# Kernel tuning notes

Measured on AMD Instinct MI355X. Metric: run time of the kernel, lower is better.

## Reference

```python
import jax, jax.numpy as jnp
import numpy as np

H = 768        # spanbert_out
WF = 20        # width_encoding_feature_size
MSW = 10       # max_span_width
TOP_RATIO = 0.4
MAX_ANTE = 50
DEPTH = 2      # coref_depth
D = 3 * H + WF # span_rep_size = 2324
NEG = -1e30


def setup_inputs() -> dict:
    key = jax.random.key(0)
    ks = jax.random.split(key, 12)
    W, G = 2048, 100
    seq = jax.random.normal(ks[0], (W, H), jnp.float32)
    sentence_map = jnp.sort(jax.random.randint(ks[1], (W,), 0, 64))
    gold_starts = jax.random.randint(ks[2], (G,), 0, W)
    gold_ends = jnp.clip(gold_starts + jax.random.randint(ks[3], (G,), 0, MSW), 0, W - 1)
    cluster_ids = jax.random.randint(ks[4], (G,), 0, 20)
    s = 0.02
    return {
        "sequence_output": seq,
        "W_alpha": jax.random.normal(ks[5], (H, 1), jnp.float32) * s,
        "b_alpha": jnp.zeros((1,), jnp.float32),
        "W_m": jax.random.normal(ks[6], (D, 1), jnp.float32) * s,
        "b_m": jnp.zeros((1,), jnp.float32),
        "W_c": jax.random.normal(ks[7], (D, D), jnp.float32) * s,
        "W_a": jax.random.normal(ks[8], (3 * D, 1), jnp.float32) * s,
        "b_a": jnp.zeros((1,), jnp.float32),
        "W_f": jax.random.normal(ks[9], (2 * D, D), jnp.float32) * s,
        "b_f": jnp.zeros((D,), jnp.float32),
        "width_feats": jax.random.normal(ks[10], (MSW, WF), jnp.float32) * s,
        "sentence_map": sentence_map,
        "gold_starts": gold_starts,
        "gold_ends": gold_ends,
        "cluster_ids": cluster_ids,
    }


def _forward(seq, W_alpha, b_alpha, W_m, b_m, W_c, W_a, b_a, W_f, b_f, width_feats,
             sentence_map, gold_starts, gold_ends, cluster_ids):
    W = seq.shape[0]
    # candidate spans: [W, MSW] -> flat [N], N = W*MSW
    cs = jnp.broadcast_to(jnp.arange(W)[:, None], (W, MSW)).reshape(-1)
    ce = (jnp.arange(W)[:, None] + jnp.arange(MSW)[None, :]).reshape(-1)
    ce_c = jnp.minimum(ce, W - 1)
    valid = (ce < W) & (sentence_map[cs] == sentence_map[ce_c])  # [N]

    # candidate cluster labels (get_candidate_labels): sum cluster ids of exact gold matches
    same_span = (cs[:, None] == gold_starts[None, :]) & (ce_c[:, None] == gold_ends[None, :])
    cand_cluster = jnp.sum(jnp.where(same_span, cluster_ids[None, :], 0), axis=1)  # [N]

    # span representations
    start_emb = seq[cs]                               # [N,H]
    end_emb = seq[ce_c]                               # [N,H]
    alphas = (seq @ W_alpha + b_alpha)[:, 0]          # [W]
    doc_range = jnp.arange(W)[None, :]
    mmask = (doc_range >= cs[:, None]) & (doc_range <= ce_c[:, None])  # [N,W]
    attn = jax.nn.softmax(jnp.where(mmask, alphas[None, :], NEG), axis=1)
    span_emb = attn @ seq                             # [N,H]
    widths = jnp.clip(ce_c - cs, 0, MSW - 1)          # width - 1
    rep = jnp.concatenate([start_emb, end_emb, span_emb, width_feats[widths]], axis=1)  # [N,D]

    # mention scoring + top-m pruning (masked_select replaced by -inf masking)
    mention_scores = (rep @ W_m + b_m)[:, 0]          # [N]
    masked_scores = jnp.where(valid, mention_scores, NEG)
    m = int(TOP_RATIO * W)
    _, top_idx = jax.lax.top_k(masked_scores, m)
    top_idx = jnp.sort(top_idx)
    top_rep = rep[top_idx]                            # [m,D]
    ts, te = cs[top_idx], ce_c[top_idx]
    tscore = mention_scores[top_idx]
    tcluster = cand_cluster[top_idx]

    # prune antecedents
    k = min(m, MAX_ANTE)
    offsets = jnp.arange(m)[:, None] - jnp.arange(m)[None, :]
    amask = offsets >= 1
    fast = tscore[:, None] + tscore[None, :] + jnp.where(amask, 0.0, NEG)
    fast = fast + (top_rep @ W_c) @ top_rep.T         # [m,m]
    _, top_ante = jax.lax.top_k(fast, k)              # [m,k]
    ta_mask = jnp.take_along_axis(amask, top_ante, axis=1)
    ta_fast = jnp.take_along_axis(fast, top_ante, axis=1)

    # iterative attention-weighted antecedent aggregation with gated update
    dummy = jnp.zeros((m, 1), seq.dtype)
    reps = top_rep
    scores_a = ta_fast
    for _ in range(DEPTH):
        ante_emb = reps[top_ante]                     # [m,k,D]
        tgt = reps[:, None, :]
        pair = jnp.concatenate(
            [jnp.broadcast_to(tgt, (m, k, D)), ante_emb, ante_emb * tgt], axis=2)  # [m,k,3D]
        slow = (pair @ W_a)[:, :, 0] + b_a[0]         # [m,k]
        scores_a = ta_fast + slow
        wts = jax.nn.softmax(jnp.concatenate([dummy, scores_a], axis=1), axis=1)  # [m,k+1]
        full = jnp.concatenate([reps[:, None, :], ante_emb], axis=1)              # [m,k+1,D]
        attended = jnp.sum(wts[:, :, None] * full, axis=1)                        # [m,D]
        f = jax.nn.sigmoid(jnp.concatenate([reps, attended], axis=1) @ W_f + b_f)
        reps = f * attended + (1.0 - f) * reps

    final_scores = jnp.concatenate([dummy, scores_a], axis=1)  # [m,k+1]

    # antecedent labels and marginal log-likelihood loss
    ante_cluster = jnp.where(ta_mask, tcluster[top_ante], -1)
    pairwise = (ante_cluster == tcluster[:, None]) & (tcluster > 0)[:, None]
    dummy_lab = ~jnp.any(pairwise, axis=1, keepdims=True)
    lab = jnp.concatenate([dummy_lab, pairwise], axis=1)
    gold_scores = jnp.where(lab, final_scores, NEG)
    loss = jnp.sum(jax.nn.logsumexp(final_scores, axis=1) - jax.nn.logsumexp(gold_scores, axis=1))
    return ts, te, top_ante, final_scores, loss


def reference(sequence_output, W_alpha, b_alpha, W_m, b_m, W_c, W_a, b_a, W_f, b_f,
              width_feats, sentence_map, gold_starts, gold_ends, cluster_ids):
    return _forward(sequence_output, W_alpha, b_alpha, W_m, b_m, W_c, W_a, b_a,
                    W_f, b_f, width_feats, sentence_map, gold_starts, gold_ends, cluster_ids)
```

## Files before the change

kernel.cpp:

```cpp
#include <hip/hip_runtime.h>
#include <cfloat>
#include <climits>
#include <math.h>

#define HD   768
#define MSW  10
#define WFK  20
#define DD   2324
#define K2   50
#define NEGF (-1e30f)

#define KPAD 2432
#define KAW  4864
#define MPAD 896
#define NPAD 2432

typedef __attribute__((ext_vector_type(8))) short    s8b;
typedef __attribute__((ext_vector_type(8))) unsigned short u16x8;
typedef __attribute__((ext_vector_type(4))) float    f32x4;

__device__ inline unsigned short f2bf(float f){
  unsigned u = __float_as_uint(f);
  unsigned r = (u + 0x7FFFu + ((u >> 16) & 1u)) >> 16;
  return (unsigned short)r;
}
__device__ inline float bf2f(unsigned short h){
  return __uint_as_float(((unsigned)h) << 16);
}

__device__ __forceinline__ void gload16(const unsigned short* g, void* l){
  __builtin_amdgcn_global_load_lds(
      (const __attribute__((address_space(1))) void*)g,
      (__attribute__((address_space(3))) void*)l, 16, 0, 0);
}

__device__ __forceinline__ int swz_col(int row, int col){
  return col ^ ((row & 7) << 3);
}

__global__ void row_proj(const float* __restrict__ seq, const float* __restrict__ Wa,
                         const float* __restrict__ ba, const float* __restrict__ Wm,
                         float* alphas, float* p1, float* p2, float* p3, int W){
  int w = blockIdx.x; int tid = threadIdx.x;
  const float* row = seq + (size_t)w * HD;
  float s0=0.f, s1=0.f, s2=0.f, s3=0.f;
  for(int h=tid; h<HD; h+=256){
    float x = row[h];
    s0 += x * Wa[h];
    s1 += x * Wm[h];
    s2 += x * Wm[HD + h];
    s3 += x * Wm[2*HD + h];
  }
  __shared__ float r0[256], r1[256], r2[256], r3[256];
  r0[tid]=s0; r1[tid]=s1; r2[tid]=s2; r3[tid]=s3;
  __syncthreads();
  for(int st=128; st>0; st>>=1){
    if(tid<st){ r0[tid]+=r0[tid+st]; r1[tid]+=r1[tid+st]; r2[tid]+=r2[tid+st]; r3[tid]+=r3[tid+st]; }
    __syncthreads();
  }
  if(tid==0){ alphas[w]=r0[0]+ba[0]; p1[w]=r1[0]; p2[w]=r2[0]; p3[w]=r3[0]; }
}

__global__ void mention_kernel(const float* __restrict__ alphas, const float* __restrict__ p1,
                               const float* __restrict__ p2, const float* __restrict__ p3,
                               const float* __restrict__ wfeat, const float* __restrict__ Wm,
                               const float* __restrict__ bm,
                               const int* __restrict__ smap, const int* __restrict__ gs,
                               const int* __restrict__ ge, const int* __restrict__ cid, int G,
                               float* mscore, float* mmask, int* ccl, int W){
  int c = blockIdx.x*blockDim.x + threadIdx.x;
  int C = W * MSW;
  if(c >= C) return;
  int s = c / MSW, r = c - s*MSW;
  int e = s + r; int ec = min(e, W-1);
  int L = ec - s;
  bool valid = (e < W) && (smap[s] == smap[ec]);
  float maxa = -FLT_MAX;
  for(int j=0;j<=L;j++) maxa = fmaxf(maxa, alphas[s+j]);
  float sum=0.f, sdot=0.f;
  for(int j=0;j<=L;j++){ float ee = expf(alphas[s+j]-maxa); sum += ee; sdot += ee*p3[s+j]; }
  sdot /= sum;
  float wp=0.f;
  for(int f=0; f<WFK; f++) wp += wfeat[L*WFK+f] * Wm[3*HD+f];
  float ms = p1[s] + p2[ec] + sdot + wp + bm[0];
  mscore[c] = ms;
  mmask[c]  = valid ? ms : NEGF;
  int cc = 0;
  for(int g=0; g<G; g++) if(s==gs[g] && ec==ge[g]) cc += cid[g];
  ccl[c] = cc;
}

__device__ inline unsigned fkey(float f){
  unsigned b = __float_as_uint(f);
  return (b & 0x80000000u) ? ~b : (b | 0x80000000u);
}

__global__ __launch_bounds__(1024)
void select_kernel(const float* __restrict__ mmask, const float* __restrict__ mscore,
                   const int* __restrict__ ccl, int m, int C, int W,
                   int* top_idx, float* tscore, int* tclust,
                   float* out_ts, float* out_te){
  const int T = 1024;
  int tid = threadIdx.x;
  int chunk = (C + T - 1)/T;
  int lo = tid*chunk, hi = min(lo+chunk, C);
  int n = hi - lo; if(n < 0) n = 0;
  unsigned kb[32];
  for(int t=0;t<n;t++) kb[t] = fkey(mmask[lo+t]);

  __shared__ unsigned s_hist[256];
  __shared__ unsigned s_scan[1024];
  __shared__ unsigned s_pref;
  __shared__ int s_rem;
  if(tid==0){ s_pref=0u; s_rem=m; }
  __syncthreads();

  for(int b=3;b>=0;b--){
    if(tid<256) s_hist[tid]=0u;
    __syncthreads();
    unsigned pref = s_pref;
    unsigned msk = (b==3)?0u:(0xFFFFFFFFu << ((b+1)*8));
    for(int t=0;t<n;t++){
      unsigned u = kb[t];
      if((u & msk)==pref) atomicAdd(&s_hist[(u>>(b*8))&0xFFu], 1u);
    }
    __syncthreads();
    if(tid==0){
      int rem = s_rem; unsigned acc=0u; int bin;
      for(bin=255;bin>=1;bin--){
        unsigned h = s_hist[bin];
        if(acc + h >= (unsigned)rem) break;
        acc += h;
      }
      if(bin < 0) bin = 0;
      s_pref = pref | ((unsigned)bin << (b*8));
      s_rem = rem - (int)acc;
    }
    __syncthreads();
  }
  unsigned Tk = s_pref;
  int need = s_rem;

  unsigned nG=0, nE=0;
  for(int t=0;t<n;t++){ unsigned u=kb[t]; nG += (u>Tk)?1u:0u; nE += (u==Tk)?1u:0u; }

  s_scan[tid]=nE; __syncthreads();
  for(int off=1; off<T; off<<=1){
    unsigned x = (tid>=off)? s_scan[tid-off]:0u; __syncthreads();
    s_scan[tid]+=x; __syncthreads();
  }
  unsigned eqBase = s_scan[tid]-nE;
  __syncthreads();

  int takeLeft = need - (int)eqBase;
  int take = takeLeft<0?0:(takeLeft>(int)nE?(int)nE:takeLeft);
  unsigned selCnt = nG + (unsigned)take;

  s_scan[tid]=selCnt; __syncthreads();
  for(int off=1; off<T; off<<=1){
    unsigned x = (tid>=off)? s_scan[tid-off]:0u; __syncthreads();
    s_scan[tid]+=x; __syncthreads();
  }
  unsigned posBase = s_scan[tid]-selCnt;

  int pos = (int)posBase; int eq = (int)eqBase;
  for(int t=0;t<n;t++){
    unsigned u = kb[t];
    bool sel = false;
    if(u>Tk) sel=true;
    else if(u==Tk){ if(eq<need) sel=true; eq++; }
    if(sel){
      int c = lo+t;
      top_idx[pos] = c;
      int s = c/MSW, r = c - s*MSW; int e = min(s + r, W-1);
      tscore[pos] = mscore[c];
      tclust[pos] = ccl[c];
      out_ts[pos] = (float)s;
      out_te[pos] = (float)e;
      pos++;
    }
  }
}

__global__ void build_rep(const float* __restrict__ seq, const float* __restrict__ alphas,
                          const float* __restrict__ wfeat, const int* __restrict__ top_idx,
                          float* rep, int W){
  int i = blockIdx.x; int tid = threadIdx.x;
  int c = top_idx[i];
  int s = c/MSW, r = c - s*MSW; int ec = min(s + r, W-1); int L = ec - s;
  float wv[MSW];
  float maxa = -FLT_MAX;
  for(int j=0;j<=L;j++) maxa = fmaxf(maxa, alphas[s+j]);
  float sum = 0.f;
  for(int j=0;j<=L;j++){ wv[j] = expf(alphas[s+j]-maxa); sum += wv[j]; }
  float inv = 1.f/sum;
  float* o = rep + (size_t)i*DD;
  for(int d=tid; d<HD; d+=256){
    o[d]      = seq[(size_t)s*HD + d];
    o[HD+d]   = seq[(size_t)ec*HD + d];
    float sp = 0.f;
    for(int j=0;j<=L;j++) sp += wv[j]*seq[(size_t)(s+j)*HD + d];
    o[2*HD+d] = sp*inv;
  }
  for(int f=tid; f<WFK; f+=256) o[3*HD+f] = wfeat[L*WFK+f];
}

__global__ void zero_buf(float* __restrict__ p, int n){
  int i = blockIdx.x*256 + threadIdx.x;
  if(i < n) p[i] = 0.f;
}

__global__ void conv_split(const float* __restrict__ src, int rows, int cols,
                           unsigned short* __restrict__ hi, unsigned short* __restrict__ lo){
  int idx = blockIdx.x*256 + threadIdx.x;
  if(idx >= MPAD*KPAD) return;
  int row = idx / KPAD, col = idx - row*KPAD;
  float v = (row < rows && col < cols) ? src[(size_t)row*cols + col] : 0.f;
  unsigned short h = f2bf(v);
  int w = row*KPAD + swz_col(row, col);
  hi[w] = h;
  lo[w] = f2bf(v - bf2f(h));
}

__global__ void conv_split_wcT(const float* __restrict__ Wc,
                               unsigned short* __restrict__ WtH, unsigned short* __restrict__ WtL){
  int n  = blockIdx.y*64 + threadIdx.x;
  int k8 = blockIdx.x*8;
  u16x8 vh, vl;
  #pragma unroll
  for(int j=0;j<8;j++){
    int k = k8 + j;
    float f = (n < DD && k < DD) ? Wc[(size_t)k*DD + n] : 0.f;
    unsigned short h = f2bf(f);
    vh[j] = h;
    vl[j] = f2bf(f - bf2f(h));
  }
  int k8s = swz_col(n, k8);
  *(u16x8*)(WtH + (size_t)n*KPAD + k8s) = vh;
  *(u16x8*)(WtL + (size_t)n*KPAD + k8s) = vl;
}

__global__ void conv_slow_ops(const float* __restrict__ cur, const float* __restrict__ Wa3,
                              unsigned short* __restrict__ CurBf, unsigned short* __restrict__ Xbf,
                              int m){
  int idx = blockIdx.x*256 + threadIdx.x;
  if(idx >= MPAD*KPAD) return;
  int row = idx / KPAD, col = idx - row*KPAD;
  float v = 0.f, w = 0.f;
  if(row < m && col < DD){ v = cur[(size_t)row*DD + col]; w = Wa3[2*DD + col]; }
  int ws = row*KPAD + swz_col(row, col);
  CurBf[ws] = f2bf(v);
  Xbf[ws]   = f2bf(v * w);
}

__global__ __launch_bounds__(256,2)
void gemm_split3_sk(const unsigned short* __restrict__ Ah, const unsigned short* __restrict__ Al,
                    const unsigned short* __restrict__ Bth, const unsigned short* __restrict__ Btl,
                    float* __restrict__ C, int M, int N, int ldc){
  __shared__ __align__(16) unsigned short sAh[128*64];
  __shared__ __align__(16) unsigned short sAl[128*64];
  __shared__ __align__(16) unsigned short sBh[128*64];
  __shared__ __align__(16) unsigned short sBl[128*64];
  int t = threadIdx.x;
  int row0 = blockIdx.y*128, col0 = blockIdx.x*128;
  const int tiles = KPAD/64;
  int per = (tiles + (int)gridDim.z - 1)/(int)gridDim.z;
  int tb = min((int)blockIdx.z*per, tiles), te = min(tb + per, tiles);
  if(tb >= te) return;
  int lane = t&63, w = t>>6;
  int wr = (w>>1)*64, wc = (w&1)*64;
  int quad = lane>>4, l15 = lane&15;
  int seg = lane&7;
  size_t ro = (size_t)(w*8 + (lane>>3));
  const unsigned short* gAh = Ah  + ((size_t)row0 + ro)*KPAD + seg*8;
  const unsigned short* gAl = Al  + ((size_t)row0 + ro)*KPAD + seg*8;
  const unsigned short* gBh = Bth + ((size_t)col0 + ro)*KPAD + seg*8;
  const unsigned short* gBl = Btl + ((size_t)col0 + ro)*KPAD + seg*8;
  const int lds0 = (w*8)*64;
  const int c0 = ((quad ^ (l15 & 7)) << 3);

  f32x4 acc[4][4];
  #pragma unroll
  for(int mi=0;mi<4;mi++)
    #pragma unroll
    for(int ni=0;ni<4;ni++) acc[mi][ni] = (f32x4){0.f,0.f,0.f,0.f};

  for(int kt=tb; kt<te; ++kt){
    size_t k0 = (size_t)kt*64;
    #pragma unroll
    for(int r=0;r<4;r++){
      size_t go = (size_t)(r*32)*KPAD + k0;
      int lo = lds0 + r*32*64;
      gload16(gAh + go, sAh + lo);
      gload16(gAl + go, sAl + lo);
      gload16(gBh + go, sBh + lo);
      gload16(gBl + go, sBl + lo);
    }
    __syncthreads();
    #pragma unroll
    for(int ks=0;ks<2;ks++){
      const int co = c0 ^ (ks<<5);
      s8b fah[4], fal[4], fbh[4], fbl[4];
      #pragma unroll
      for(int mi=0;mi<4;mi++){
        int ra = (wr+mi*16+l15)*64 + co;
        fah[mi] = *(const s8b*)&sAh[ra];
        fal[mi] = *(const s8b*)&sAl[ra];
      }
      #pragma unroll
      for(int ni=0;ni<4;ni++){
        int rb = (wc+ni*16+l15)*64 + co;
        fbh[ni] = *(const s8b*)&sBh[rb];
        fbl[ni] = *(const s8b*)&sBl[rb];
      }
      #pragma unroll
      for(int mi=0;mi<4;mi++)
        #pragma unroll
        for(int ni=0;ni<4;ni++){
          acc[mi][ni] = __builtin_amdgcn_mfma_f32_16x16x32_bf16(fah[mi], fbh[ni], acc[mi][ni], 0,0,0);
          acc[mi][ni] = __builtin_amdgcn_mfma_f32_16x16x32_bf16(fah[mi], fbl[ni], acc[mi][ni], 0,0,0);
          acc[mi][ni] = __builtin_amdgcn_mfma_f32_16x16x32_bf16(fal[mi], fbh[ni], acc[mi][ni], 0,0,0);
        }
    }
    __syncthreads();
  }

  #pragma unroll
  for(int ni=0;ni<4;ni++){
    int gn = col0 + wc + ni*16 + l15;
    if(gn >= N) continue;
    #pragma unroll
    for(int mi=0;mi<4;mi++){
      #pragma unroll
      for(int rg=0;rg<4;rg++){
        int gr = row0 + wr + mi*16 + quad*4 + rg;
        if(gr >= M) continue;
        atomicAdd(&C[(size_t)gr*ldc + gn], acc[mi][ni][rg]);
      }
    }
  }
}

__global__ __launch_bounds__(256,2)
void gemm_bf16_m97(const unsigned short* __restrict__ A, const unsigned short* __restrict__ Bt,
                   float* __restrict__ C, int M, int N, int ldc, int ldk, int tiles){
  __shared__ __align__(16) unsigned short sA[2][128*64];
  __shared__ __align__(16) unsigned short sB[2][128*64];
  int t = threadIdx.x;
  int row0 = blockIdx.y*128, col0 = blockIdx.x*128;
  int per = (tiles + (int)gridDim.z - 1)/(int)gridDim.z;
  int tb = min((int)blockIdx.z*per, tiles), te = min(tb + per, tiles);
  if(tb >= te) return;
  int lane = t&63, w = t>>6;
  int wr = (w>>1)*64, wc = (w&1)*64;
  int quad = lane>>4, l15 = lane&15;
  int seg = lane&7;
  size_t ro = (size_t)(w*8 + (lane>>3));
  const unsigned short* gA = A  + ((size_t)row0 + ro)*ldk + seg*8;
  const unsigned short* gB = Bt + ((size_t)col0 + ro)*ldk + seg*8;
  const int lds0 = (w*8)*64;
  const int c0 = ((quad ^ (l15 & 7)) << 3);

  f32x4 acc[4][4];
  #pragma unroll
  for(int mi=0;mi<4;mi++)
    #pragma unroll
    for(int ni=0;ni<4;ni++) acc[mi][ni] = (f32x4){0.f,0.f,0.f,0.f};

  auto STAGE = [&](int b, int kt){
    size_t k0 = (size_t)kt*64;
    #pragma unroll
    for(int r=0;r<4;r++){
      size_t go = (size_t)(r*32)*ldk + k0;
      int lo = lds0 + r*32*64;
      gload16(gA + go, &sA[b][lo]);
      gload16(gB + go, &sB[b][lo]);
    }
  };

  STAGE(0, tb);
  __syncthreads();
  int buf = 0;
  for(int kt=tb; kt<te; ++kt){
    if(kt+1 < te) STAGE(buf^1, kt+1);
    #pragma unroll
    for(int ks=0;ks<2;ks++){
      const int co = c0 ^ (ks<<5);
      s8b fa[4], fb[4];
      #pragma unroll
      for(int mi=0;mi<4;mi++) fa[mi] = *(const s8b*)&sA[buf][(wr+mi*16+l15)*64 + co];
      #pragma unroll
      for(int ni=0;ni<4;ni++) fb[ni] = *(const s8b*)&sB[buf][(wc+ni*16+l15)*64 + co];
      #pragma unroll
      for(int mi=0;mi<4;mi++)
        #pragma unroll
        for(int ni=0;ni<4;ni++)
          acc[mi][ni] = __builtin_amdgcn_mfma_f32_16x16x32_bf16(fa[mi], fb[ni], acc[mi][ni], 0,0,0);
    }
    __syncthreads();
    buf ^= 1;
  }

  #pragma unroll
  for(int ni=0;ni<4;ni++){
    int gn = col0 + wc + ni*16 + l15;
    if(gn >= N) continue;
    #pragma unroll
    for(int mi=0;mi<4;mi++){
      #pragma unroll
      for(int rg=0;rg<4;rg++){
        int gr = row0 + wr + mi*16 + quad*4 + rg;
        if(gr >= M) continue;
        atomicAdd(&C[(size_t)gr*ldc + gn], acc[mi][ni][rg]);
      }
    }
  }
}

#define NT 13
__global__ void topante_kernel(const float* __restrict__ tscore, const float* __restrict__ bilin,
                               int m, int* ante, float* tafast, float* out_ante){
  int i = blockIdx.x; int lane = threadIdx.x;
  float tsi = tscore[i];
  float v[NT];
  #pragma unroll
  for(int t=0;t<NT;t++){
    int j = lane + t*64;
    float f = -FLT_MAX;
    if(j < m){
      f = tsi + tscore[j];
      f += (j < i) ? 0.f : NEGF;
      f += bilin[(size_t)i*m + j];
    }
    v[t] = f;
  }
  unsigned consumed = 0u;
  int r_ante = 0; float r_fast = 0.f;
  for(int it=0; it<K2; ++it){
    float lv = -FLT_MAX; int li = m;
    #pragma unroll
    for(int t=0;t<NT;t++){
      bool live = ((consumed >> t) & 1u) == 0u;
      if(live && v[t] > lv){ lv = v[t]; li = lane + t*64; }
    }
    float bv = lv; int bi = li;
    #pragma unroll
    for(int off=32; off>0; off>>=1){
      float ov = __shfl_xor(bv, off);
      int   oi = __shfl_xor(bi, off);
      if(ov > bv || (ov == bv && oi < bi)){ bv = ov; bi = oi; }
    }
    if(bi < m && (bi & 63) == lane) consumed |= (1u << (bi >> 6));
    if(lane == it){ r_ante = bi; r_fast = bv; }
  }
  if(lane < K2){
    ante[(size_t)i*K2 + lane]   = r_ante;
    tafast[(size_t)i*K2 + lane] = r_fast;
    out_ante[(size_t)i*K2+lane] = (float)r_ante;
  }
}

__global__ void uv_kernel(const float* __restrict__ reps, const float* __restrict__ Wa3,
                          float* u, float* v, int m){
  int i = blockIdx.x; int tid = threadIdx.x;
  const float* rp = reps + (size_t)i*DD;
  float s1=0.f, s2=0.f;
  for(int d=tid; d<DD; d+=256){ float x = rp[d]; s1 += x*Wa3[d]; s2 += x*Wa3[DD+d]; }
  __shared__ float r1[256], r2[256];
  r1[tid]=s1; r2[tid]=s2; __syncthreads();
  for(int st=128; st>0; st>>=1){
    if(tid<st){ r1[tid]+=r1[tid+st]; r2[tid]+=r2[tid+st]; }
    __syncthreads();
  }
  if(tid==0){ u[i]=r1[0]; v[i]=r2[0]; }
}

__global__ void slow_gather(const float* __restrict__ P, const float* __restrict__ u,
                            const float* __restrict__ v, const int* __restrict__ ante,
                            const float* __restrict__ tafast, const float* __restrict__ ba,
                            float* sc, int m){
  int p = blockIdx.x*256 + threadIdx.x;
  if(p >= m*K2) return;
  int i = p / K2; int j = ante[p];
  sc[p] = tafast[p] + u[i] + v[j] + P[(size_t)i*m + j] + ba[0];
}

__global__ void attend_kernel(const float* __restrict__ reps, const float* __restrict__ sc,
                              const int* __restrict__ ante, float* att, int m){
  int i = blockIdx.x; int tid = threadIdx.x;
  __shared__ float wts[K2+1];
  __shared__ float scs[K2];
  __shared__ int   js[K2];
  if(tid < K2){ scs[tid] = sc[(size_t)i*K2 + tid]; js[tid] = ante[(size_t)i*K2 + tid]; }
  __syncthreads();
  if(tid==0){
    float mx = 0.f;
    for(int t=0;t<K2;t++) mx = fmaxf(mx, scs[t]);
    float sum = expf(0.f - mx); wts[0] = sum;
    for(int t=0;t<K2;t++){ float e = expf(scs[t]-mx); wts[t+1]=e; sum += e; }
    float inv = 1.f/sum;
    for(int t=0;t<=K2;t++) wts[t] *= inv;
  }
  __syncthreads();
  const float* ri_ = reps + (size_t)i*DD;
  for(int d=tid; d<DD; d+=256){
    float a = wts[0]*ri_[d];
    for(int t=0;t<K2;t++) a += wts[t+1]*reps[(size_t)js[t]*DD + d];
    att[(size_t)i*DD + d] = a;
  }
}

__global__ void conv_acat(const float* __restrict__ cur, const float* __restrict__ att,
                          unsigned short* __restrict__ A, int m){
  int idx = blockIdx.x*256 + threadIdx.x;
  if(idx >= MPAD*KAW) return;
  int row = idx / KAW, col = idx - row*KAW;
  float v = 0.f;
  if(row < m){
    if(col < DD) v = cur[(size_t)row*DD + col];
    else if(col >= KPAD && col < KPAD + DD) v = att[(size_t)row*DD + (col - KPAD)];
  }
  A[row*KAW + swz_col(row, col)] = f2bf(v);
}

__global__ void conv_wf(const float* __restrict__ Wf, unsigned short* __restrict__ Bt){
  int n  = blockIdx.y*64 + threadIdx.x;
  int k8 = blockIdx.x*8;
  int s  = (k8 >= KPAD) ? 1 : 0;
  int kk = k8 - s*KPAD;
  u16x8 v;
  #pragma unroll
  for(int j=0;j<8;j++){
    int k = kk + j;
    float f = (n < DD && k < DD) ? Wf[(size_t)(s*DD + k)*DD + n] : 0.f;
    v[j] = f2bf(f);
  }
  int k8s = swz_col(n, k8);
  *(u16x8*)(Bt + (size_t)n*KAW + k8s) = v;
}

__global__ void gate_update(const float* __restrict__ bfv, const float* __restrict__ att,
                            const float* __restrict__ cur, float* __restrict__ nxt, int total){
  int idx = blockIdx.x*256 + threadIdx.x;
  if(idx >= total) return;
  int col = idx % DD;
  float pre = nxt[idx] + bfv[col];
  float g = 1.f/(1.f + expf(-pre));
  nxt[idx] = g*att[idx] + (1.f - g)*cur[idx];
}

__global__ void final_loss(const float* __restrict__ sc, const int* __restrict__ ante,
                           const int* __restrict__ tclust, float* out_fs, float* row_loss, int m){
  int i = blockIdx.x*blockDim.x + threadIdx.x;
  if(i >= m) return;
  int tci = tclust[i];
  unsigned long long labm = 0ull;
  bool anyp = false;
  float mx = 0.f;
  float mg = -FLT_MAX;
  for(int t=0;t<K2;t++){
    float v = sc[(size_t)i*K2 + t];
    mx = fmaxf(mx, v);
    int j = ante[(size_t)i*K2 + t];
    bool mk = (j < i);
    int ac = mk ? tclust[j] : -1;
    bool p = (ac == tci) && (tci > 0);
    if(p){ labm |= (1ull << (t+1)); anyp = true; mg = fmaxf(mg, v); }
  }
  if(!anyp){ labm |= 1ull; mg = 0.f; }
  float s1 = expf(0.f - mx);
  float s2 = (labm & 1ull) ? expf(0.f - mg) : 0.f;
  float* o = out_fs + (size_t)i*(K2+1);
  o[0] = 0.f;
  for(int t=0;t<K2;t++){
    float v = sc[(size_t)i*K2 + t];
    o[t+1] = v;
    s1 += expf(v - mx);
    if(labm & (1ull << (t+1))) s2 += expf(v - mg);
  }
  row_loss[i] = (mx + logf(s1)) - (mg + logf(s2));
}

__global__ void loss_sum(const float* __restrict__ row_loss, float* out, int m){
  int tid = threadIdx.x;
  float s = 0.f;
  for(int i=tid; i<m; i+=256) s += row_loss[i];
  __shared__ float red[256];
  red[tid]=s; __syncthreads();
  for(int st=128; st>0; st>>=1){ if(tid<st) red[tid]+=red[tid+st]; __syncthreads(); }
  if(tid==0) out[0] = red[0];
}

extern "C" void kernel_launch(void* const* d_in, const int* in_sizes, int n_in,
                              void* d_out, int out_size, void* d_ws, size_t ws_size,
                              hipStream_t stream){
  const int W = in_sizes[11];
  const int G = in_sizes[12];
  const int C = W * MSW;
  const int m = (int)(0.4 * (double)W);

  const float* seq   = (const float*)d_in[0];
  const float* Wal   = (const float*)d_in[1];
  const float* bal   = (const float*)d_in[2];
  const float* Wm    = (const float*)d_in[3];
  const float* bm    = (const float*)d_in[4];
  const float* Wc    = (const float*)d_in[5];
  const float* WaA   = (const float*)d_in[6];
  const float* baA   = (const float*)d_in[7];
  const float* Wf    = (const float*)d_in[8];
  const float* bf    = (const float*)d_in[9];
  const float* wfeat = (const float*)d_in[10];
  const int*   smap  = (const int*)d_in[11];
  const int*   gs    = (const int*)d_in[12];
  const int*   ge    = (const int*)d_in[13];
  const int*   cid   = (const int*)d_in[14];
  float* out = (float*)d_out;

  char* ws = (char*)d_ws;
  size_t off = 0;
  auto alloc = [&](size_t bytes)->char*{
    char* p = ws + off;
    off += (bytes + 255) & ~(size_t)255;
    return p;
  };
  const size_t PLANE  = (size_t)MPAD*KPAD*2;
  const size_t WPLANE = (size_t)NPAD*KPAD*2;

  float* alphas  = (float*)alloc((size_t)W*4);
  float* p1      = (float*)alloc((size_t)W*4);
  float* p2      = (float*)alloc((size_t)W*4);
  float* p3      = (float*)alloc((size_t)W*4);
  float* mscore  = (float*)alloc((size_t)C*4);
  float* mmask   = (float*)alloc((size_t)C*4);
  int*   ccl     = (int*)  alloc((size_t)C*4);
  int*   top_idx = (int*)  alloc((size_t)m*4);
  float* tscore  = (float*)alloc((size_t)m*4);
  int*   tclust  = (int*)  alloc((size_t)m*4);
  float* B1      = (float*)alloc((size_t)m*DD*4);
  float* B2      = (float*)alloc((size_t)m*DD*4);
  float* B3      = (float*)alloc((size_t)m*DD*4);
  float* bilin   = (float*)alloc((size_t)m*m*4);
  int*   ante    = (int*)  alloc((size_t)m*K2*4);
  float* tafast  = (float*)alloc((size_t)m*K2*4);
  float* uB      = (float*)alloc((size_t)m*4);
  float* vB      = (float*)alloc((size_t)m*4);
  float* scB     = (float*)alloc((size_t)m*K2*4);
  float* rloss   = (float*)alloc((size_t)m*4);
  char* regionA = alloc(2*PLANE);
  unsigned short* RepH  = (unsigned short*)regionA;
  unsigned short* RepL  = (unsigned short*)(regionA + PLANE);
  unsigned short* XbfA  = (unsigned short*)regionA;
  unsigned short* CurBf = (unsigned short*)(regionA + PLANE);
  unsigned short* Acat  = (unsigned short*)regionA;
  char* regionB = alloc(2*WPLANE);
  unsigned short* WtH  = (unsigned short*)regionB;
  unsigned short* WtL  = (unsigned short*)(regionB + WPLANE);
  unsigned short* A2H  = (unsigned short*)regionB;
  unsigned short* A2L  = (unsigned short*)(regionB + PLANE);
  unsigned short* BtWf = (unsigned short*)regionB;

  float* out_ts   = out;
  float* out_te   = out + m;
  float* out_ante = out + 2*m;
  float* out_fs   = out + 2*m + (size_t)m*K2;
  float* out_loss = out + 2*m + (size_t)m*K2 + (size_t)m*(K2+1);

  row_proj<<<W, 256, 0, stream>>>(seq, Wal, bal, Wm, alphas, p1, p2, p3, W);
  mention_kernel<<<(C+255)/256, 256, 0, stream>>>(alphas, p1, p2, p3, wfeat, Wm, bm,
                                                  smap, gs, ge, cid, G,
                                                  mscore, mmask, ccl, W);
  select_kernel<<<1, 1024, 0, stream>>>(mmask, mscore, ccl, m, C, W,
                                        top_idx, tscore, tclust, out_ts, out_te);
  build_rep<<<m, 256, 0, stream>>>(seq, alphas, wfeat, top_idx, B1, W);
  {
    const int NEL = MPAD*KPAD;
    conv_split<<<(NEL+255)/256, 256, 0, stream>>>(B1, m, DD, RepH, RepL);
    dim3 gw(KPAD/8, NPAD/64);
    conv_split_wcT<<<gw, 64, 0, stream>>>(Wc, WtH, WtL);
    zero_buf<<<(m*DD+255)/256, 256, 0, stream>>>(B2, m*DD);
    dim3 g1(NPAD/128, MPAD/128, 3);
    gemm_split3_sk<<<g1, 256, 0, stream>>>(RepH, RepL, WtH, WtL, B2, m, DD, DD);
    conv_split<<<(NEL+255)/256, 256, 0, stream>>>(B2, m, DD, A2H, A2L);
    zero_buf<<<(m*m+255)/256, 256, 0, stream>>>(bilin, m*m);
    dim3 g2(MPAD/128, MPAD/128, 10);
    gemm_split3_sk<<<g2, 256, 0, stream>>>(A2H, A2L, RepH, RepL, bilin, m, m, m);
  }
  topante_kernel<<<m, 64, 0, stream>>>(tscore, bilin, m, ante, tafast, out_ante);
  {
    dim3 g(KAW/8, NPAD/64);
    conv_wf<<<g, 64, 0, stream>>>(Wf, BtWf);
  }

  float* cur = B1; float* nxt = B2;
  const int NEL = MPAD*KPAD;
  const int total = m * DD;
  for(int depth=0; depth<2; depth++){
    uv_kernel<<<m, 256, 0, stream>>>(cur, WaA, uB, vB, m);
    conv_slow_ops<<<(NEL+255)/256, 256, 0, stream>>>(cur, WaA, CurBf, XbfA, m);
    zero_buf<<<(m*m+255)/256, 256, 0, stream>>>(bilin, m*m);
    dim3 gp(MPAD/128, MPAD/128, 10);
    gemm_bf16_m97<<<gp, 256, 0, stream>>>(XbfA, CurBf, bilin, m, m, m, KPAD, KPAD/64);
    slow_gather<<<(m*K2+255)/256, 256, 0, stream>>>(bilin, uB, vB, ante, tafast, baA, scB, m);
    attend_kernel<<<m, 256, 0, stream>>>(cur, scB, ante, B3, m);
    conv_acat<<<(MPAD*KAW+255)/256, 256, 0, stream>>>(cur, B3, Acat, m);
    zero_buf<<<(total+255)/256, 256, 0, stream>>>(nxt, total);
    dim3 gg(NPAD/128, MPAD/128, 3);
    gemm_bf16_m97<<<gg, 256, 0, stream>>>(Acat, BtWf, nxt, m, DD, DD, KAW, KAW/64);
    gate_update<<<(total+255)/256, 256, 0, stream>>>(bf, B3, cur, nxt, total);
    float* t = cur; cur = nxt; nxt = t;
  }

  final_loss<<<(m+255)/256, 256, 0, stream>>>(scB, ante, tclust, out_fs, rloss, m);
  loss_sum<<<1, 256, 0, stream>>>(rloss, out_loss, m);
}
```

Before: 843.2 us.

## Double-buffer split-bf16 GEMM LDS tiles with 32-wide K and new swizzle

Splits the K tile from 64 to 32 and double-buffers the LDS staging, so the async global-to-LDS loads for the next tile are issued before the MFMA work on the current one. The LDS swizzle and the matching operand conversion kernels change to a 32-column pattern. This aims to hide global load latency behind compute, at the cost of twice as many loop iterations and barriers, and possible LDS bank conflicts if the new swizzle does not spread the accesses well. Only one barrier per iteration remains, so correctness depends on the async loads completing before that barrier.

```diff
diff --git a/kernel.cpp b/kernel.cpp
--- a/kernel.cpp
+++ b/kernel.cpp
@@ -36,6 +36,9 @@
 
 __device__ __forceinline__ int swz_col(int row, int col){
   return col ^ ((row & 7) << 3);
+}
+__device__ __forceinline__ int swz32(int row, int col){
+  return col ^ (((row >> 1) & 3) << 3);
 }
 
 __global__ void row_proj(const float* __restrict__ seq, const float* __restrict__ Wa,
@@ -217,7 +220,7 @@
   int row = idx / KPAD, col = idx - row*KPAD;
   float v = (row < rows && col < cols) ? src[(size_t)row*cols + col] : 0.f;
   unsigned short h = f2bf(v);
-  int w = row*KPAD + swz_col(row, col);
+  int w = row*KPAD + swz32(row, col);
   hi[w] = h;
   lo[w] = f2bf(v - bf2f(h));
 }
@@ -235,7 +238,7 @@
     vh[j] = h;
     vl[j] = f2bf(f - bf2f(h));
   }
-  int k8s = swz_col(n, k8);
+  int k8s = swz32(n, k8);
   *(u16x8*)(WtH + (size_t)n*KPAD + k8s) = vh;
   *(u16x8*)(WtL + (size_t)n*KPAD + k8s) = vl;
 }
@@ -257,27 +260,25 @@
 void gemm_split3_sk(const unsigned short* __restrict__ Ah, const unsigned short* __restrict__ Al,
                     const unsigned short* __restrict__ Bth, const unsigned short* __restrict__ Btl,
                     float* __restrict__ C, int M, int N, int ldc){
-  __shared__ __align__(16) unsigned short sAh[128*64];
-  __shared__ __align__(16) unsigned short sAl[128*64];
-  __shared__ __align__(16) unsigned short sBh[128*64];
-  __shared__ __align__(16) unsigned short sBl[128*64];
+  __shared__ __align__(16) unsigned short sAh[2][128*32];
+  __shared__ __align__(16) unsigned short sAl[2][128*32];
+  __shared__ __align__(16) unsigned short sBh[2][128*32];
+  __shared__ __align__(16) unsigned short sBl[2][128*32];
   int t = threadIdx.x;
   int row0 = blockIdx.y*128, col0 = blockIdx.x*128;
-  const int tiles = KPAD/64;
+  const int tiles = KPAD/32;
   int per = (tiles + (int)gridDim.z - 1)/(int)gridDim.z;
   int tb = min((int)blockIdx.z*per, tiles), te = min(tb + per, tiles);
   if(tb >= te) return;
   int lane = t&63, w = t>>6;
   int wr = (w>>1)*64, wc = (w&1)*64;
   int quad = lane>>4, l15 = lane&15;
-  int seg = lane&7;
-  size_t ro = (size_t)(w*8 + (lane>>3));
-  const unsigned short* gAh = Ah  + ((size_t)row0 + ro)*KPAD + seg*8;
-  const unsigned short* gAl = Al  + ((size_t)row0 + ro)*KPAD + seg*8;
-  const unsigned short* gBh = Bth + ((size_t)col0 + ro)*KPAD + seg*8;
-  const unsigned short* gBl = Btl + ((size_t)col0 + ro)*KPAD + seg*8;
-  const int lds0 = (w*8)*64;
-  const int c0 = ((quad ^ (l15 & 7)) << 3);
+  size_t ro = (size_t)(w*16 + (lane>>2));
+  const unsigned short* gAh = Ah  + ((size_t)row0 + ro)*KPAD + (lane&3)*8;
+  const unsigned short* gAl = Al  + ((size_t)row0 + ro)*KPAD + (lane&3)*8;
+  const unsigned short* gBh = Bth + ((size_t)col0 + ro)*KPAD + (lane&3)*8;
+  const unsigned short* gBl = Btl + ((size_t)col0 + ro)*KPAD + (lane&3)*8;
+  const int lds0 = (w*16)*32;
 
   f32x4 acc[4][4];
   #pragma unroll
@@ -285,44 +286,49 @@
     #pragma unroll
     for(int ni=0;ni<4;ni++) acc[mi][ni] = (f32x4){0.f,0.f,0.f,0.f};
 
+  auto STAGE = [&](int b, int kt){
+    size_t k0 = (size_t)kt*32;
+    #pragma unroll
+    for(int r=0;r<2;r++){
+      size_t go = (size_t)(r*64)*KPAD + k0;
+      int lo = lds0 + r*64*32;
+      gload16(gAh + go, &sAh[b][lo]);
+      gload16(gAl + go, &sAl[b][lo]);
+      gload16(gBh + go, &sBh[b][lo]);
+      gload16(gBl + go, &sBl[b][lo]);
+    }
+  };
+
+  STAGE(0, tb);
+  __syncthreads();
+  int buf = 0;
   for(int kt=tb; kt<te; ++kt){
-    size_t k0 = (size_t)kt*64;
-    #pragma unroll
-    for(int r=0;r<4;r++){
-      size_t go = (size_t)(r*32)*KPAD + k0;
-      int lo = lds0 + r*32*64;
-      gload16(gAh + go, sAh + lo);
-      gload16(gAl + go, sAl + lo);
-      gload16(gBh + go, sBh + lo);
-      gload16(gBl + go, sBl + lo);
-    }
-    __syncthreads();
-    #pragma unroll
-    for(int ks=0;ks<2;ks++){
-      const int co = c0 ^ (ks<<5);
-      s8b fah[4], fal[4], fbh[4], fbl[4];
-      #pragma unroll
-      for(int mi=0;mi<4;mi++){
-        int ra = (wr+mi*16+l15)*64 + co;
-        fah[mi] = *(const s8b*)&sAh[ra];
-        fal[mi] = *(const s8b*)&sAl[ra];
-      }
+    if(kt+1 < te) STAGE(buf^1, kt+1);
+    s8b fah[4], fal[4], fbh[4], fbl[4];
+    #pragma unroll
+    for(int mi=0;mi<4;mi++){
+      int sr = wr+mi*16+l15;
+      int ra = sr*32 + ((quad ^ ((sr>>1)&3))<<3);
+      fah[mi] = *(const s8b*)&sAh[buf][ra];
+      fal[mi] = *(const s8b*)&sAl[buf][ra];
+    }
+    #pragma unroll
+    for(int ni=0;ni<4;ni++){
+      int sr = wc+ni*16+l15;
+      int rb = sr*32 + ((quad ^ ((sr>>1)&3))<<3);
+      fbh[ni] = *(const s8b*)&sBh[buf][rb];
+      fbl[ni] = *(const s8b*)&sBl[buf][rb];
+    }
+    #pragma unroll
+    for(int mi=0;mi<4;mi++)
       #pragma unroll
       for(int ni=0;ni<4;ni++){
-        int rb = (wc+ni*16+l15)*64 + co;
-        fbh[ni] = *(const s8b*)&sBh[rb];
-        fbl[ni] = *(const s8b*)&sBl[rb];
+        acc[mi][ni] = __builtin_amdgcn_mfma_f32_16x16x32_bf16(fah[mi], fbh[ni], acc[mi][ni], 0,0,0);
+        acc[mi][ni] = __builtin_amdgcn_mfma_f32_16x16x32_bf16(fah[mi], fbl[ni], acc[mi][ni], 0,0,0);
+        acc[mi][ni] = __builtin_amdgcn_mfma_f32_16x16x32_bf16(fal[mi], fbh[ni], acc[mi][ni], 0,0,0);
       }
-      #pragma unroll
-      for(int mi=0;mi<4;mi++)
-        #pragma unroll
-        for(int ni=0;ni<4;ni++){
-          acc[mi][ni] = __builtin_amdgcn_mfma_f32_16x16x32_bf16(fah[mi], fbh[ni], acc[mi][ni], 0,0,0);
-          acc[mi][ni] = __builtin_amdgcn_mfma_f32_16x16x32_bf16(fah[mi], fbl[ni], acc[mi][ni], 0,0,0);
-          acc[mi][ni] = __builtin_amdgcn_mfma_f32_16x16x32_bf16(fal[mi], fbh[ni], acc[mi][ni], 0,0,0);
-        }
-    }
     __syncthreads();
+    buf ^= 1;
   }
 
   #pragma unroll
```

New measurement: 851.5 us. No clear change (+1.0%).
